# Kernel tuning notes

Hardware: AMD Instinct MI355X
Metric: run time of the kernel (lower is better)

The kernel has to match this reference:

```python
import math
import jax, jax.numpy as jnp
import numpy as np

# ---- module hyperparams (from init_kwargs defaults) ----
NUM_AA, EMB_DIM, K, EXCLUDE = 20, 16, 64, 2
R_ON, R_CUT, DELTA, WALL = 8.0, 10.0, 0.3, 10.0
RHO_MIN, RHO_MAX, RHO_BASE = 1.6, 2.8, 2.0
B, L = 8, 2048
BIG = 1e9  # masks excluded pairs in the distance matrix


def setup_inputs() -> dict:
    key = jax.random.key(0)
    k1, k2, k3 = jax.random.split(key, 3)
    # coordinates scaled to a realistic Angstrom spread so switch/softplus are exercised
    R = jax.random.normal(k1, (B, L, 3), dtype=jnp.float32) * 10.0
    seq = jax.random.randint(k2, (B, L), 0, NUM_AA, dtype=jnp.int64)
    # learned params: AA embedding table + size head (small random weight, bias at rho_base)
    emb_table = jax.random.normal(k3, (NUM_AA, EMB_DIM), dtype=jnp.float32)
    size_w = 0.1 * jax.random.normal(jax.random.fold_in(key, 7), (1, EMB_DIM), dtype=jnp.float32)
    frac = (RHO_BASE - RHO_MIN) / max(1e-6, RHO_MAX - RHO_MIN)
    frac = min(0.999, max(0.001, frac))
    size_b = jnp.full((1,), math.log(frac / (1.0 - frac)), dtype=jnp.float32)
    return {"R": R, "seq": seq, "emb_table": emb_table, "size_w": size_w, "size_b": size_b}


def _rho(s, emb_table, size_w, size_b):
    # per-residue learned radius in [RHO_MIN, RHO_MAX]; s: int indices, any shape
    e = emb_table[s]                                  # (..., EMB_DIM)
    x = jnp.einsum('...d,d->...', e, size_w[0]) + size_b[0]
    return RHO_MIN + (RHO_MAX - RHO_MIN) * jax.nn.sigmoid(x)


def _smooth_switch(r):
    # smoothstep from 1 (r<=R_ON) down to 0 (r>=R_CUT)
    t = jnp.clip((r - R_ON) / (R_CUT - R_ON), 0.0, 1.0)
    return 1.0 - t * t * (3.0 - 2.0 * t)


def reference(R, seq, emb_table, size_w, size_b):
    b, l, _ = R.shape
    # pairwise distances (B, L, L)
    diff = R[:, :, None, :] - R[:, None, :, :]
    D = jnp.sqrt(jnp.maximum(jnp.sum(diff * diff, axis=-1), 1e-12))
    # exclude bonded/near-diagonal pairs |i-j| <= EXCLUDE (includes self)
    idx = jnp.arange(l)
    excl = jnp.abs(idx[:, None] - idx[None, :]) <= EXCLUDE
    Dm = jnp.where(excl[None], BIG, D)
    # K smallest distances per residue -> negate for lax.top_k
    neg_r, j = jax.lax.top_k(-Dm, K)                  # (B, L, K)
    r = -neg_r
    # gather neighbor sequence ids along L
    seq_j = jnp.take_along_axis(jnp.broadcast_to(seq[:, :, None], (b, l, K)), j, axis=1)
    # pair radius r0_ij = rho(s_i) + rho(s_j)
    rho_i = _rho(seq, emb_table, size_w, size_b)[:, :, None]   # (B, L, 1)
    rho_j = _rho(seq_j, emb_table, size_w, size_b)             # (B, L, K)
    r0 = rho_i + rho_j
    rep = WALL * jax.nn.softplus((r0 - r) / (DELTA + 1e-12))
    return (rep * _smooth_switch(r)).sum(axis=(1, 2))          # (B,)
```

## Files before the change

### kernel.cpp

```cpp
#include <hip/hip_runtime.h>
#include <hip/hip_fp16.h>
#include <math.h>

#define LRES 2048
#define NB 8
#define KSEL 64
#define EMBD 16
#define NBIN 128
#define BINSCALE 1.28f
#define BINW 0.78125f
#define NSLOT 16

__global__ void prep_kernel(const float* __restrict__ R,
                            const int* __restrict__ seq,
                            const float* __restrict__ emb,
                            const float* __restrict__ w,
                            const float* __restrict__ bias,
                            uint2* __restrict__ pts) {
    int idx = blockIdx.x * blockDim.x + threadIdx.x;
    if (idx < NB * LRES) {
        int s = seq[idx];
        float x = bias[0];
#pragma unroll
        for (int d = 0; d < EMBD; ++d) x += emb[s * EMBD + d] * w[d];
        float rho = 1.6f + 1.2f / (1.0f + expf(-x));
        __half2 h0 = __floats2half2_rn(R[idx * 3 + 0], R[idx * 3 + 1]);
        __half2 h1 = __floats2half2_rn(R[idx * 3 + 2], rho);
        pts[idx] = make_uint2(*(unsigned*)&h0, *(unsigned*)&h1);
    }
}

#define LDS_FENCE() asm volatile("s_waitcnt lgkmcnt(0)" ::: "memory")

__global__ __launch_bounds__(256) void repel_kernel(const uint2* __restrict__ pts,
                                                    float* __restrict__ partial) {
    const int w    = threadIdx.x >> 6;
    const int lane = threadIdx.x & 63;
    const int row  = blockIdx.x * 4 + w;
    const int b    = row >> 11;
    const int i    = row & 2047;

    __shared__ unsigned hist[4][NBIN];
    __shared__ unsigned slots[4][NSLOT][64];
    __shared__ unsigned shT[4];

    const uint2* __restrict__ P = pts + (b << 11);
    const uint4* __restrict__ P4 = (const uint4*)P;

    *(uint2*)&hist[w][lane << 1] = make_uint2(0u, 0u);
    if (lane == 0) shT[w] = NBIN - 1;

    float2 cc0 = __half22float2(*(__half2*)&P[i].x);
    float2 cc1 = __half22float2(*(__half2*)&P[i].y);
    const float cx = cc0.x, cy = cc0.y, cz = cc1.x, rho_i = cc1.y;
    LDS_FENCE();

    unsigned d2u[32];
#pragma unroll
    for (int t = 0; t < 16; ++t) {
        uint4 u = P4[(t << 6) + lane];
        int j0 = (t << 7) + (lane << 1);
        {
            float2 f0 = __half22float2(*(__half2*)&u.x);
            float2 f1 = __half22float2(*(__half2*)&u.y);
            float dx = f0.x - cx, dy = f0.y - cy, dz = f1.x - cz;
            float d2 = dx * dx + dy * dy + dz * dz;
            int dij = j0 - i; dij = (dij < 0) ? -dij : dij;
            unsigned du = (dij <= 2) ? 0xFFFFFFFFu : __float_as_uint(d2);
            d2u[2 * t] = du;
            if (du <= 0x42C7FFFFu)
                atomicAdd(&hist[w][(unsigned)(d2 * BINSCALE)], 1u);
        }
        {
            float2 f0 = __half22float2(*(__half2*)&u.z);
            float2 f1 = __half22float2(*(__half2*)&u.w);
            float dx = f0.x - cx, dy = f0.y - cy, dz = f1.x - cz;
            float d2 = dx * dx + dy * dy + dz * dz;
            int dij = j0 + 1 - i; dij = (dij < 0) ? -dij : dij;
            unsigned du = (dij <= 2) ? 0xFFFFFFFFu : __float_as_uint(d2);
            d2u[2 * t + 1] = du;
            if (du <= 0x42C7FFFFu)
                atomicAdd(&hist[w][(unsigned)(d2 * BINSCALE)], 1u);
        }
    }
    LDS_FENCE();

    uint2 hv = *(const uint2*)&hist[w][lane << 1];
    unsigned p = hv.x + hv.y;
    unsigned s = p;
#pragma unroll
    for (int o = 1; o < 64; o <<= 1) {
        unsigned u = __shfl_up(s, o, 64);
        if (lane >= o) s += u;
    }
    unsigned e0 = s - p;
    if (s >= KSEL && e0 < KSEL) {
        unsigned sub = (e0 + hv.x >= KSEL) ? 0u : 1u;
        shT[w] = (lane << 1) + sub;
    }
    LDS_FENCE();
    const unsigned T = shT[w];
    const unsigned tkb = __float_as_uint((float)(T + 1) * BINW);

    unsigned cnt = 0;
#pragma unroll
    for (int m = 0; m < 32; ++m) {
        if (d2u[m] < tkb && cnt < NSLOT) {
            unsigned j = (unsigned)(((m >> 1) << 7) | (m & 1)) + ((unsigned)lane << 1);
            slots[w][cnt][lane] = (d2u[m] & 0xFFFFF800u) | j;
            ++cnt;
        }
    }
    LDS_FENCE();

    float acc = 0.0f;
    for (unsigned k = 0; k < cnt; ++k) {
        unsigned key = slots[w][k][lane];
        unsigned j = key & 2047u;
        float d2 = __uint_as_float(key & 0xFFFFF800u);
        float r = __fsqrt_rn(fmaxf(d2, 1e-12f));
        uint2 pj = P[j];
        float rho_j = __high2float(*(__half2*)&pj.y);
        float x = (rho_i + rho_j - r) * (1.0f / 0.3f);
        float sp = fmaxf(x, 0.0f) + __logf(1.0f + __expf(-fabsf(x)));
        float t = fminf(fmaxf((r - 8.0f) * 0.5f, 0.0f), 1.0f);
        float sw = 1.0f - t * t * (3.0f - 2.0f * t);
        acc += 10.0f * sp * sw;
    }
#pragma unroll
    for (int o = 32; o > 0; o >>= 1) acc += __shfl_down(acc, o, 64);
    if (lane == 0) partial[row] = acc;
}

__global__ void reduce_kernel(const float* __restrict__ partial, float* __restrict__ out) {
    __shared__ float sh[4];
    const int b = blockIdx.x;
    const int tid = threadIdx.x;
    float acc = 0.0f;
#pragma unroll
    for (int k = 0; k < 8; ++k) acc += partial[(b << 11) + (k << 8) + tid];
#pragma unroll
    for (int o = 32; o > 0; o >>= 1) acc += __shfl_down(acc, o, 64);
    if ((tid & 63) == 0) sh[tid >> 6] = acc;
    __syncthreads();
    if (tid == 0) out[b] = sh[0] + sh[1] + sh[2] + sh[3];
}

extern "C" void kernel_launch(void* const* d_in, const int* in_sizes, int n_in,
                              void* d_out, int out_size, void* d_ws, size_t ws_size,
                              hipStream_t stream) {
    const float* R    = (const float*)d_in[0];
    const int*   seq  = (const int*)d_in[1];
    const float* emb  = (const float*)d_in[2];
    const float* w    = (const float*)d_in[3];
    const float* bias = (const float*)d_in[4];
    float* out = (float*)d_out;

    uint2* pts     = (uint2*)d_ws;
    float* partial = (float*)((char*)d_ws + NB * LRES * sizeof(uint2));

    prep_kernel<<<(NB * LRES + 255) / 256, 256, 0, stream>>>(R, seq, emb, w, bias, pts);
    repel_kernel<<<NB * LRES / 4, 256, 0, stream>>>(pts, partial);
    reduce_kernel<<<NB, 256, 0, stream>>>(partial, out);
}
```

Measured before the change: 89.54 us.

## Stage full-precision batch points in LDS and drop fp16 packing

Each 512-thread block now loads its batch's full fp32 coordinates and rho into a 32 KB LDS array and computes distances from LDS instead of reading fp16-packed points from global memory. The prep kernel only computes rho. Blocks grow to eight rows and NSLOT drops from 16 to 8. This removes repeated global or L2 reads per row and the half-precision rounding, at the cost of each block reloading the whole batch into LDS, which limits occupancy. The smaller slot cap raises the risk of dropping neighbours on a lane.

```diff
diff --git a/kernel.cpp b/kernel.cpp
--- a/kernel.cpp
+++ b/kernel.cpp
@@ -1,5 +1,4 @@
 #include <hip/hip_runtime.h>
-#include <hip/hip_fp16.h>
 #include <math.h>
 
 #define LRES 2048
@@ -9,79 +8,71 @@
 #define NBIN 128
 #define BINSCALE 1.28f
 #define BINW 0.78125f
-#define NSLOT 16
+#define NSLOT 8
 
-__global__ void prep_kernel(const float* __restrict__ R,
-                            const int* __restrict__ seq,
-                            const float* __restrict__ emb,
-                            const float* __restrict__ w,
-                            const float* __restrict__ bias,
-                            uint2* __restrict__ pts) {
+__global__ void rho_kernel(const int* __restrict__ seq,
+                           const float* __restrict__ emb,
+                           const float* __restrict__ w,
+                           const float* __restrict__ bias,
+                           float* __restrict__ rho) {
     int idx = blockIdx.x * blockDim.x + threadIdx.x;
     if (idx < NB * LRES) {
         int s = seq[idx];
         float x = bias[0];
 #pragma unroll
         for (int d = 0; d < EMBD; ++d) x += emb[s * EMBD + d] * w[d];
-        float rho = 1.6f + 1.2f / (1.0f + expf(-x));
-        __half2 h0 = __floats2half2_rn(R[idx * 3 + 0], R[idx * 3 + 1]);
-        __half2 h1 = __floats2half2_rn(R[idx * 3 + 2], rho);
-        pts[idx] = make_uint2(*(unsigned*)&h0, *(unsigned*)&h1);
+        rho[idx] = 1.6f + 1.2f / (1.0f + expf(-x));
     }
 }
 
 #define LDS_FENCE() asm volatile("s_waitcnt lgkmcnt(0)" ::: "memory")
 
-__global__ __launch_bounds__(256) void repel_kernel(const uint2* __restrict__ pts,
-                                                    float* __restrict__ partial) {
+__global__ __launch_bounds__(512, 8) void repel_kernel(const float* __restrict__ R,
+                                                       const float* __restrict__ rho,
+                                                       float* __restrict__ partial) {
     const int w    = threadIdx.x >> 6;
     const int lane = threadIdx.x & 63;
-    const int row  = blockIdx.x * 4 + w;
+    const int row  = blockIdx.x * 8 + w;
     const int b    = row >> 11;
     const int i    = row & 2047;
 
-    __shared__ unsigned hist[4][NBIN];
-    __shared__ unsigned slots[4][NSLOT][64];
-    __shared__ unsigned shT[4];
+    __shared__ float4  pt[LRES];
+    __shared__ unsigned hist[8][NBIN];
+    __shared__ unsigned slots[8][NSLOT][64];
+    __shared__ unsigned shT[8];
 
-    const uint2* __restrict__ P = pts + (b << 11);
-    const uint4* __restrict__ P4 = (const uint4*)P;
-
+    {
+        const float4* Rg = (const float4*)(R + (size_t)b * (LRES * 3));
+        const float4* Qg = (const float4*)(rho + (b << 11));
+        int t = threadIdx.x;
+        float4 f0 = Rg[3 * t + 0];
+        float4 f1 = Rg[3 * t + 1];
+        float4 f2 = Rg[3 * t + 2];
+        float4 q  = Qg[t];
+        pt[4 * t + 0] = make_float4(f0.x, f0.y, f0.z, q.x);
+        pt[4 * t + 1] = make_float4(f0.w, f1.x, f1.y, q.y);
+        pt[4 * t + 2] = make_float4(f1.z, f1.w, f2.x, q.z);
+        pt[4 * t + 3] = make_float4(f2.y, f2.z, f2.w, q.w);
+    }
     *(uint2*)&hist[w][lane << 1] = make_uint2(0u, 0u);
     if (lane == 0) shT[w] = NBIN - 1;
+    __syncthreads();
 
-    float2 cc0 = __half22float2(*(__half2*)&P[i].x);
-    float2 cc1 = __half22float2(*(__half2*)&P[i].y);
-    const float cx = cc0.x, cy = cc0.y, cz = cc1.x, rho_i = cc1.y;
-    LDS_FENCE();
+    float4 c = pt[i];
+    const float cx = c.x, cy = c.y, cz = c.z, rho_i = c.w;
 
     unsigned d2u[32];
-#pragma unroll
-    for (int t = 0; t < 16; ++t) {
-        uint4 u = P4[(t << 6) + lane];
-        int j0 = (t << 7) + (lane << 1);
-        {
-            float2 f0 = __half22float2(*(__half2*)&u.x);
-            float2 f1 = __half22float2(*(__half2*)&u.y);
-            float dx = f0.x - cx, dy = f0.y - cy, dz = f1.x - cz;
-            float d2 = dx * dx + dy * dy + dz * dz;
-            int dij = j0 - i; dij = (dij < 0) ? -dij : dij;
-            unsigned du = (dij <= 2) ? 0xFFFFFFFFu : __float_as_uint(d2);
-            d2u[2 * t] = du;
-            if (du <= 0x42C7FFFFu)
-                atomicAdd(&hist[w][(unsigned)(d2 * BINSCALE)], 1u);
-        }
-        {
-            float2 f0 = __half22float2(*(__half2*)&u.z);
-            float2 f1 = __half22float2(*(__half2*)&u.w);
-            float dx = f0.x - cx, dy = f0.y - cy, dz = f1.x - cz;
-            float d2 = dx * dx + dy * dy + dz * dz;
-            int dij = j0 + 1 - i; dij = (dij < 0) ? -dij : dij;
-            unsigned du = (dij <= 2) ? 0xFFFFFFFFu : __float_as_uint(d2);
-            d2u[2 * t + 1] = du;
-            if (du <= 0x42C7FFFFu)
-                atomicAdd(&hist[w][(unsigned)(d2 * BINSCALE)], 1u);
-        }
+#pragma unroll 8
+    for (int t = 0; t < 32; ++t) {
+        int j = (t << 6) + lane;
+        float4 p = pt[j];
+        float dx = p.x - cx, dy = p.y - cy, dz = p.z - cz;
+        float d2 = dx * dx + dy * dy + dz * dz;
+        int dij = j - i; dij = (dij < 0) ? -dij : dij;
+        unsigned du = (dij <= 2) ? 0xFFFFFFFFu : __float_as_uint(d2);
+        d2u[t] = du;
+        if (du <= 0x42C7FFFFu)
+            atomicAdd(&hist[w][(unsigned)(d2 * BINSCALE)], 1u);
     }
     LDS_FENCE();
 
@@ -99,15 +90,15 @@
         shT[w] = (lane << 1) + sub;
     }
     LDS_FENCE();
-    const unsigned T = shT[w];
+    const unsigned T   = shT[w];
     const unsigned tkb = __float_as_uint((float)(T + 1) * BINW);
 
     unsigned cnt = 0;
 #pragma unroll
-    for (int m = 0; m < 32; ++m) {
-        if (d2u[m] < tkb && cnt < NSLOT) {
-            unsigned j = (unsigned)(((m >> 1) << 7) | (m & 1)) + ((unsigned)lane << 1);
-            slots[w][cnt][lane] = (d2u[m] & 0xFFFFF800u) | j;
+    for (int t = 0; t < 32; ++t) {
+        if (d2u[t] < tkb && cnt < NSLOT) {
+            unsigned j = (unsigned)((t << 6) + lane);
+            slots[w][cnt][lane] = (d2u[t] & 0xFFFFF800u) | j;
             ++cnt;
         }
     }
@@ -119,8 +110,7 @@
         unsigned j = key & 2047u;
         float d2 = __uint_as_float(key & 0xFFFFF800u);
         float r = __fsqrt_rn(fmaxf(d2, 1e-12f));
-        uint2 pj = P[j];
-        float rho_j = __high2float(*(__half2*)&pj.y);
+        float rho_j = pt[j].w;
         float x = (rho_i + rho_j - r) * (1.0f / 0.3f);
         float sp = fmaxf(x, 0.0f) + __logf(1.0f + __expf(-fabsf(x)));
         float t = fminf(fmaxf((r - 8.0f) * 0.5f, 0.0f), 1.0f);
@@ -156,10 +146,10 @@
     const float* bias = (const float*)d_in[4];
     float* out = (float*)d_out;
 
-    uint2* pts     = (uint2*)d_ws;
-    float* partial = (float*)((char*)d_ws + NB * LRES * sizeof(uint2));
+    float* rho     = (float*)d_ws;
+    float* partial = (float*)d_ws + NB * LRES;
 
-    prep_kernel<<<(NB * LRES + 255) / 256, 256, 0, stream>>>(R, seq, emb, w, bias, pts);
-    repel_kernel<<<NB * LRES / 4, 256, 0, stream>>>(pts, partial);
+    rho_kernel<<<(NB * LRES + 255) / 256, 256, 0, stream>>>(seq, emb, w, bias, rho);
+    repel_kernel<<<NB * LRES / 8, 512, 0, stream>>>(R, rho, partial);
     reduce_kernel<<<NB, 256, 0, stream>>>(partial, out);
 }
```

Measured after the change: 93.03 us. 3.9% more time.
